# Kernel tuning notes

Measured on AMD Instinct MI355X. Metric: run time of the kernel, lower is better.

The kernel has to match this reference:

```python
import jax, jax.numpy as jnp
import numpy as np

B, C, H, W = 4, 256, 64, 64
CI = 128  # inter_channels = in_channels // 2
EPS = 1e-5  # torch BatchNorm default eps


def setup_inputs() -> dict:
    key = jax.random.key(0)
    ks = jax.random.split(key, 8)

    def w(k, shape, s=0.02):
        return jax.random.normal(k, shape, jnp.float32) * s

    return {
        "x": jax.random.normal(ks[0], (B, C, H, W), jnp.float32),
        # theta (Q) linear + BatchNorm1d (inference-mode running stats)
        "theta_w": w(ks[1], (CI, C)), "theta_b": jnp.zeros((CI,), jnp.float32),
        "theta_bn_gamma": jnp.ones((CI,), jnp.float32), "theta_bn_beta": jnp.zeros((CI,), jnp.float32),
        "theta_bn_mean": jnp.zeros((CI,), jnp.float32), "theta_bn_var": jnp.ones((CI,), jnp.float32),
        # phi (K) linear + BatchNorm1d
        "phi_w": w(ks[2], (CI, C)), "phi_b": jnp.zeros((CI,), jnp.float32),
        "phi_bn_gamma": jnp.ones((CI,), jnp.float32), "phi_bn_beta": jnp.zeros((CI,), jnp.float32),
        "phi_bn_mean": jnp.zeros((CI,), jnp.float32), "phi_bn_var": jnp.ones((CI,), jnp.float32),
        # g (V) linear
        "g_w": w(ks[3], (CI, C)), "g_b": jnp.zeros((CI,), jnp.float32),
        # W_z output linear
        "wz_w": w(ks[4], (C, CI)), "wz_b": jnp.zeros((C,), jnp.float32),
        # output BatchNorm2d (gamma nonzero instead of init-0 so output is non-trivial)
        "bn_gamma": w(ks[5], (C,), 0.1), "bn_beta": jnp.zeros((C,), jnp.float32),
        "bn_mean": jnp.zeros((C,), jnp.float32), "bn_var": jnp.ones((C,), jnp.float32),
    }


def _linear(z, w, b):
    # z: [B, N, C], w: [D, C] -> [B, N, D]
    return jnp.einsum('bnc,dc->bnd', z, w) + b


def _bn(z, gamma, beta, mean, var):
    # per-channel affine BN in inference mode, channel on last axis
    return (z - mean) * jax.lax.rsqrt(var + EPS) * gamma + beta


def reference(x, theta_w, theta_b, theta_bn_gamma, theta_bn_beta, theta_bn_mean, theta_bn_var,
              phi_w, phi_b, phi_bn_gamma, phi_bn_beta, phi_bn_mean, phi_bn_var,
              g_w, g_b, wz_w, wz_b, bn_gamma, bn_beta, bn_mean, bn_var):
    b, c, h, w = x.shape
    n = h * w
    ci = theta_w.shape[0]
    scale = float(ci) ** (-0.5)

    x_flat = x.reshape(b, c, n).transpose(0, 2, 1)  # [B, N, C]
    Q = _bn(_linear(x_flat, theta_w, theta_b), theta_bn_gamma, theta_bn_beta, theta_bn_mean, theta_bn_var)
    K = _bn(_linear(x_flat, phi_w, phi_b), phi_bn_gamma, phi_bn_beta, phi_bn_mean, phi_bn_var)
    V = _linear(x_flat, g_w, g_b)  # [B, N, CI]

    # attention computed in fp32 (matches torch amp-disabled block)
    attn = jnp.einsum('bnd,bmd->bnm', Q.astype(jnp.float32), K.astype(jnp.float32)) * scale
    attn = jax.nn.softmax(attn, axis=-1).astype(V.dtype)  # [B, N, N]

    y = jnp.einsum('bnm,bmd->bnd', attn, V)  # [B, N, CI]
    y = jnp.einsum('bnd,cd->bnc', y, wz_w) + wz_b  # [B, N, C]
    y = y.transpose(0, 2, 1).reshape(b, c, h, w)

    # BatchNorm2d (inference mode), channel axis 1
    rstd = jax.lax.rsqrt(bn_var + EPS)
    y = (y - bn_mean[None, :, None, None]) * (rstd * bn_gamma)[None, :, None, None] + bn_beta[None, :, None, None]
    return y + x
```

## Files before the change

### kernel.cpp

```cpp
#include <hip/hip_runtime.h>
#include <stdint.h>

typedef __attribute__((ext_vector_type(8))) short bf16x8;
typedef __attribute__((ext_vector_type(4))) float f32x4;

#define WS_WQKV   0u
#define WS_WZ     196608u
#define WS_SCL    262144u
#define WS_SHF    263680u
#define WS_WZS    265216u
#define WS_WZT    266240u
#define WS_Q      524288u
#define WS_K      (WS_Q  + 4194304u)
#define WS_VT     (WS_K  + 4194304u)
#define WS_Y      (WS_VT + 4194304u)
#define WS_OP     (WS_Y  + 4194304u)
#define WS_LP     (WS_OP + 16777216u)

__device__ __forceinline__ short f2bf(float f) {
  union { float f; uint32_t u; } v; v.f = f;
  uint32_t r = v.u + 0x7fffu + ((v.u >> 16) & 1u);
  return (short)(r >> 16);
}

__device__ __forceinline__ uint32_t pack2_bf16(float a, float b) {
  union { float f; uint32_t u; } x, y; x.f = a; y.f = b;
  return ((y.u + 0x8000u) & 0xffff0000u) | ((x.u + 0x8000u) >> 16);
}

__device__ __forceinline__ f32x4 mfma16(bf16x8 a, bf16x8 b, f32x4 c) {
  return __builtin_amdgcn_mfma_f32_16x16x32_bf16(a, b, c, 0, 0, 0);
}

__device__ __forceinline__ void load_lds16(const short* gp, short* lp) {
  __builtin_amdgcn_global_load_lds(
      (const __attribute__((address_space(1))) uint32_t*)gp,
      (__attribute__((address_space(3))) uint32_t*)lp, 16, 0, 0);
}

__global__ __launch_bounds__(256) void prep_kernel(
    const float* theta_w, const float* phi_w, const float* g_w, const float* wz_w,
    const float* theta_b, const float* tg, const float* tb, const float* tm, const float* tv,
    const float* phi_b,   const float* pg, const float* pb, const float* pm, const float* pv,
    const float* g_b,
    const float* wz_b, const float* bg, const float* bb, const float* bm, const float* bv,
    char* ws) {
  int idx = blockIdx.x * 256 + threadIdx.x;
  short* wqkv = (short*)(ws + WS_WQKV);
  if (idx < 98304) {
    float w;
    if (idx < 32768) w = theta_w[idx];
    else if (idx < 65536) w = phi_w[idx - 32768];
    else w = g_w[idx - 65536];
    wqkv[idx] = f2bf(w);
  }
  if (idx < 32768) ((short*)(ws + WS_WZ))[idx] = f2bf(wz_w[idx]);
  if (idx < 384) {
    float s, t;
    if (idx < 128)      { s = tg[idx] * rsqrtf(tv[idx] + 1e-5f);
                          t = (theta_b[idx] - tm[idx]) * s + tb[idx]; }
    else if (idx < 256) { int d = idx - 128; s = pg[d] * rsqrtf(pv[d] + 1e-5f);
                          t = (phi_b[d] - pm[d]) * s + pb[d]; }
    else                { int d = idx - 256; s = 1.0f; t = g_b[d]; }
    ((float*)(ws + WS_SCL))[idx] = s;
    ((float*)(ws + WS_SHF))[idx] = t;
  }
  if (idx < 256) {
    float s = bg[idx] * rsqrtf(bv[idx] + 1e-5f);
    float t = (wz_b[idx] - bm[idx]) * s + bb[idx];
    ((float*)(ws + WS_WZS))[idx] = s;
    ((float*)(ws + WS_WZT))[idx] = t;
  }
}

__global__ __launch_bounds__(256) void qkv_kernel(const float* __restrict__ x, char* ws) {
  const int nt2 = blockIdx.x, b = blockIdx.y;
  const int t = threadIdx.x;
  __shared__ __attribute__((aligned(16))) short xs[32][264];
  const short* wqkv = (const short*)(ws + WS_WQKV);
  const float* scl = (const float*)(ws + WS_SCL);
  const float* shf = (const float*)(ws + WS_SHF);
  const int n0 = nt2 * 32;
  #pragma unroll
  for (int i = 0; i < 8; ++i) {
    int chunk = i * 256 + t;
    int c = chunk >> 3, n4 = chunk & 7;
    const float4 v = *(const float4*)(x + ((size_t)(b * 256 + c) << 12) + n0 + n4 * 4);
    xs[n4 * 4 + 0][c] = f2bf(v.x);
    xs[n4 * 4 + 1][c] = f2bf(v.y);
    xs[n4 * 4 + 2][c] = f2bf(v.z);
    xs[n4 * 4 + 3][c] = f2bf(v.w);
  }
  __syncthreads();
  const int wv = t >> 6, l = t & 63, lr = l & 15, q = l >> 4;
  const int wn = wv & 1, dh = wv >> 1;
  bf16x8 a[8];
  #pragma unroll
  for (int kt = 0; kt < 8; ++kt) a[kt] = *(const bf16x8*)&xs[wn * 16 + lr][kt * 32 + q * 8];
  f32x4 acc[12] = {};
  #pragma unroll
  for (int kt = 0; kt < 8; ++kt) {
    #pragma unroll
    for (int s = 0; s < 12; ++s) {
      const short* wp = wqkv + (size_t)(dh * 192 + s * 16 + lr) * 256 + kt * 32 + q * 8;
      bf16x8 bf = *(const bf16x8*)wp;
      acc[s] = mfma16(a[kt], bf, acc[s]);
    }
  }
  const float s2 = 0.08838834764831845f * 1.4426950408889634f;
  #pragma unroll
  for (int s = 0; s < 12; ++s) {
    int dg = dh * 192 + s * 16 + lr;
    float sc = scl[dg], sh = shf[dg];
    if (dg < 128) { sc *= s2; sh *= s2; }
    short vals[4];
    #pragma unroll
    for (int r = 0; r < 4; ++r) vals[r] = f2bf(acc[s][r] * sc + sh);
    int nbase = n0 + wn * 16 + q * 4;
    if (dg < 128) {
      short* Q = (short*)(ws + WS_Q) + ((size_t)b << 19);
      #pragma unroll
      for (int r = 0; r < 4; ++r) Q[(size_t)(nbase + r) * 128 + dg] = vals[r];
    } else if (dg < 256) {
      int d = dg - 128;
      short* Kt = (short*)(ws + WS_K) + ((size_t)b << 19);
      int kt2 = d >> 5, qa = (d >> 3) & 3, e = d & 7;
      int tile = nbase >> 6, sg = (nbase >> 4) & 3, lr0 = nbase & 15;
      size_t base = ((size_t)((tile * 16 + sg * 4 + kt2) * 64 + qa * 16 + lr0) << 3) + e;
      #pragma unroll
      for (int r = 0; r < 4; ++r) Kt[base + r * 8] = vals[r];
    } else {
      int d = dg - 256;
      short* Vt = (short*)(ws + WS_VT) + ((size_t)b << 19);
      int dt = d >> 4, lrv = d & 15;
      int tile = nbase >> 6, mm = nbase & 63;
      int h = mm >> 5, qv = (mm >> 3) & 3, e0 = mm & 7;
      size_t base = ((size_t)((tile * 16 + dt * 2 + h) * 64 + qv * 16 + lrv) << 3) + e0;
      short4 pk; pk.x = vals[0]; pk.y = vals[1]; pk.z = vals[2]; pk.w = vals[3];
      *(short4*)(Vt + base) = pk;
    }
  }
}

__global__ __launch_bounds__(256, 2) void attn_kernel(char* ws) {
  const int g = blockIdx.x;
  const int b = (g & 7) >> 1;
  const int idx = ((g >> 3) << 1) | (g & 1);
  const int nt = idx >> 2, mc = idx & 3;
  const int t = threadIdx.x, w = t >> 6, l = t & 63, lr = l & 15, q = l >> 4;
  __shared__ __attribute__((aligned(16))) short ksl[16][512];
  __shared__ __attribute__((aligned(16))) short vsl[16][512];
  __shared__ __attribute__((aligned(16))) short psl[4][2][2][512];
  const short* Q  = (const short*)(ws + WS_Q)  + ((size_t)b << 19);
  const short* Kt = (const short*)(ws + WS_K)  + ((size_t)b << 19);
  const short* Vt = (const short*)(ws + WS_VT) + ((size_t)b << 19);
  const int n0w = nt * 128 + w * 32;
  bf16x8 qf[2][4];
  #pragma unroll
  for (int j = 0; j < 2; ++j) {
    const short* qp = Q + (size_t)(n0w + j * 16 + lr) * 128 + q * 8;
    #pragma unroll
    for (int kt = 0; kt < 4; ++kt) qf[j][kt] = *(const bf16x8*)(qp + kt * 32);
  }
  f32x4 o[2][8] = {};
  float lsum[2] = {0.f, 0.f};

  for (int it = 0; it < 16; ++it) {
    const int tile = mc * 16 + it;
    const short* kg = Kt + (size_t)tile * 8192;
    const short* vg = Vt + (size_t)tile * 8192;
    __syncthreads();
    #pragma unroll
    for (int i = 0; i < 4; ++i) {
      int gi = i * 4 + w;
      load_lds16(kg + gi * 512 + l * 8, &ksl[gi][0]);
      load_lds16(vg + gi * 512 + l * 8, &vsl[gi][0]);
    }
    __syncthreads();
    f32x4 sacc[2][4] = {};
    #pragma unroll
    for (int kt = 0; kt < 4; ++kt) {
      #pragma unroll
      for (int s = 0; s < 4; ++s) {
        bf16x8 kf = *(const bf16x8*)&ksl[s * 4 + kt][l * 8];
        sacc[0][s] = mfma16(kf, qf[0][kt], sacc[0][s]);
        sacc[1][s] = mfma16(kf, qf[1][kt], sacc[1][s]);
      }
    }
    #pragma unroll
    for (int j = 0; j < 2; ++j) {
      #pragma unroll
      for (int s = 0; s < 4; ++s) {
        float e0 = exp2f(sacc[j][s][0]);
        float e1 = exp2f(sacc[j][s][1]);
        float e2 = exp2f(sacc[j][s][2]);
        float e3 = exp2f(sacc[j][s][3]);
        lsum[j] += (e0 + e1) + (e2 + e3);
        uint2 pk;
        pk.x = pack2_bf16(e0, e1);
        pk.y = pack2_bf16(e2, e3);
        *(uint2*)&psl[w][j][s >> 1][(((s & 1) * 2 + (q >> 1)) * 16 + lr) * 8 + (q & 1) * 4] = pk;
      }
    }
    bf16x8 pf[2][2];
    #pragma unroll
    for (int j = 0; j < 2; ++j)
      #pragma unroll
      for (int h = 0; h < 2; ++h)
        pf[j][h] = *(const bf16x8*)&psl[w][j][h][l * 8];
    #pragma unroll
    for (int dt = 0; dt < 8; ++dt) {
      #pragma unroll
      for (int h = 0; h < 2; ++h) {
        bf16x8 vf = *(const bf16x8*)&vsl[dt * 2 + h][l * 8];
        o[0][dt] = mfma16(vf, pf[0][h], o[0][dt]);
        o[1][dt] = mfma16(vf, pf[1][h], o[1][dt]);
      }
    }
  }
  const int cb = mc * 4 + b;
  float* LP = (float*)(ws + WS_LP) + ((size_t)cb << 12);
  #pragma unroll
  for (int j = 0; j < 2; ++j) {
    float s = lsum[j];
    s += __shfl_xor(s, 16, 64);
    s += __shfl_xor(s, 32, 64);
    if (l < 16) LP[n0w + j * 16 + l] = s;
  }
  short* OPc = (short*)(ws + WS_OP) + ((size_t)cb << 19);
  #pragma unroll
  for (int j = 0; j < 2; ++j)
    #pragma unroll
    for (int dt = 0; dt < 8; ++dt) {
      short4 pk;
      pk.x = f2bf(o[j][dt][0]); pk.y = f2bf(o[j][dt][1]);
      pk.z = f2bf(o[j][dt][2]); pk.w = f2bf(o[j][dt][3]);
      *(short4*)&OPc[((size_t)(n0w + j * 16 + lr) << 7) + dt * 16 + q * 4] = pk;
    }
}

__global__ __launch_bounds__(256) void proj_kernel(const float* __restrict__ x,
                                                   char* ws, float* __restrict__ out) {
  const int nt = blockIdx.x, b = blockIdx.y;
  const int t = threadIdx.x, wv = t >> 6, l = t & 63, lr = l & 15, q = l >> 4;
  __shared__ __attribute__((aligned(16))) short ys[16][136];
  const short* OP = (const short*)(ws + WS_OP);
  const float* LP = (const float*)(ws + WS_LP);
  const short* WZ = (const short*)(ws + WS_WZ);
  const float* wzs = (const float*)(ws + WS_WZS);
  const float* wzt = (const float*)(ws + WS_WZT);
  const int n0 = nt * 16;
  {
    int row = t >> 4, d8 = (t & 15) * 8;
    int n = n0 + row;
    float acc8[8] = {};
    float lsf = 0.f;
    #pragma unroll
    for (int mc = 0; mc < 4; ++mc) {
      int cb = mc * 4 + b;
      const short* p = OP + ((size_t)cb << 19) + ((size_t)n << 7) + d8;
      uint4 v = *(const uint4*)p;
      uint32_t uu[4] = {v.x, v.y, v.z, v.w};
      #pragma unroll
      for (int w = 0; w < 4; ++w) {
        union { uint32_t u; float f; } lo, hi;
        lo.u = uu[w] << 16; hi.u = uu[w] & 0xffff0000u;
        acc8[w * 2 + 0] += lo.f;
        acc8[w * 2 + 1] += hi.f;
      }
      lsf += LP[(cb << 12) + n];
    }
    float inv = 1.0f / lsf;
    short out8[8];
    #pragma unroll
    for (int j = 0; j < 8; ++j) out8[j] = f2bf(acc8[j] * inv);
    *(uint4*)&ys[row][d8] = *(uint4*)out8;
  }
  __syncthreads();
  bf16x8 a[4];
  #pragma unroll
  for (int kt = 0; kt < 4; ++kt) a[kt] = *(const bf16x8*)&ys[lr][kt * 32 + q * 8];
  f32x4 acc[4] = {};
  #pragma unroll
  for (int kt = 0; kt < 4; ++kt) {
    #pragma unroll
    for (int s = 0; s < 4; ++s) {
      const short* wp = WZ + (size_t)(wv * 64 + s * 16 + lr) * 128 + kt * 32 + q * 8;
      bf16x8 bf = *(const bf16x8*)wp;
      acc[s] = mfma16(a[kt], bf, acc[s]);
    }
  }
  #pragma unroll
  for (int s = 0; s < 4; ++s) {
    int c = wv * 64 + s * 16 + lr;
    float sc = wzs[c], sh = wzt[c];
    int nbase = n0 + q * 4;
    size_t base = ((size_t)(b * 256 + c) << 12) + nbase;
    float4 xv = *(const float4*)(x + base);
    float4 ov;
    ov.x = acc[s][0] * sc + sh + xv.x;
    ov.y = acc[s][1] * sc + sh + xv.y;
    ov.z = acc[s][2] * sc + sh + xv.z;
    ov.w = acc[s][3] * sc + sh + xv.w;
    *(float4*)(out + base) = ov;
  }
}

extern "C" void kernel_launch(void* const* d_in, const int* in_sizes, int n_in,
                              void* d_out, int out_size, void* d_ws, size_t ws_size,
                              hipStream_t stream) {
  const float* x       = (const float*)d_in[0];
  const float* theta_w = (const float*)d_in[1];
  const float* theta_b = (const float*)d_in[2];
  const float* tg      = (const float*)d_in[3];
  const float* tb      = (const float*)d_in[4];
  const float* tm      = (const float*)d_in[5];
  const float* tv      = (const float*)d_in[6];
  const float* phi_w   = (const float*)d_in[7];
  const float* phi_b   = (const float*)d_in[8];
  const float* pg      = (const float*)d_in[9];
  const float* pb      = (const float*)d_in[10];
  const float* pm      = (const float*)d_in[11];
  const float* pv      = (const float*)d_in[12];
  const float* g_w     = (const float*)d_in[13];
  const float* g_b     = (const float*)d_in[14];
  const float* wz_w    = (const float*)d_in[15];
  const float* wz_b    = (const float*)d_in[16];
  const float* bg      = (const float*)d_in[17];
  const float* bb      = (const float*)d_in[18];
  const float* bm      = (const float*)d_in[19];
  const float* bv      = (const float*)d_in[20];
  char* ws = (char*)d_ws;
  float* out = (float*)d_out;

  prep_kernel<<<384, 256, 0, stream>>>(theta_w, phi_w, g_w, wz_w,
                                       theta_b, tg, tb, tm, tv,
                                       phi_b, pg, pb, pm, pv,
                                       g_b, wz_b, bg, bb, bm, bv, ws);
  qkv_kernel<<<dim3(128, 4), 256, 0, stream>>>(x, ws);
  attn_kernel<<<512, 256, 0, stream>>>(ws);
  proj_kernel<<<dim3(256, 4), 256, 0, stream>>>(x, ws, out);
}
```

Measured before the change: 196.6 us.

## Double-buffer K/V LDS tiles in attention loop and raise MFMA wave priority

The attention kernel now keeps two LDS buffers for K and V. The next tile's global-to-LDS copy is issued before computing on the current tile, with one barrier per tile instead of two, so memory latency can overlap with MFMA work. s_setprio brackets the MFMA sections to favour waves issuing matrix ops. LDS use per block grows from about 48KB to about 80KB, which may limit how many blocks fit on a CU alongside the two-blocks-per-CU launch bound.

```diff
diff --git a/kernel.cpp b/kernel.cpp
--- a/kernel.cpp
+++ b/kernel.cpp
@@ -148,8 +148,10 @@
   const int idx = ((g >> 3) << 1) | (g & 1);
   const int nt = idx >> 2, mc = idx & 3;
   const int t = threadIdx.x, w = t >> 6, l = t & 63, lr = l & 15, q = l >> 4;
-  __shared__ __attribute__((aligned(16))) short ksl[16][512];
-  __shared__ __attribute__((aligned(16))) short vsl[16][512];
+  __shared__ __attribute__((aligned(16))) short ks0[16][512];
+  __shared__ __attribute__((aligned(16))) short vs0[16][512];
+  __shared__ __attribute__((aligned(16))) short ks1[16][512];
+  __shared__ __attribute__((aligned(16))) short vs1[16][512];
   __shared__ __attribute__((aligned(16))) short psl[4][2][2][512];
   const short* Q  = (const short*)(ws + WS_Q)  + ((size_t)b << 19);
   const short* Kt = (const short*)(ws + WS_K)  + ((size_t)b << 19);
@@ -165,19 +167,23 @@
   f32x4 o[2][8] = {};
   float lsum[2] = {0.f, 0.f};
 
-  for (int it = 0; it < 16; ++it) {
-    const int tile = mc * 16 + it;
-    const short* kg = Kt + (size_t)tile * 8192;
-    const short* vg = Vt + (size_t)tile * 8192;
-    __syncthreads();
+  const short* kbase = Kt + (size_t)(mc * 16) * 8192;
+  const short* vbase = Vt + (size_t)(mc * 16) * 8192;
+
+  auto stage = [&](short (*KS)[512], short (*VS)[512], int it) {
+    const short* kg = kbase + (size_t)it * 8192;
+    const short* vg = vbase + (size_t)it * 8192;
     #pragma unroll
     for (int i = 0; i < 4; ++i) {
       int gi = i * 4 + w;
-      load_lds16(kg + gi * 512 + l * 8, &ksl[gi][0]);
-      load_lds16(vg + gi * 512 + l * 8, &vsl[gi][0]);
-    }
-    __syncthreads();
+      load_lds16(kg + gi * 512 + l * 8, &KS[gi][0]);
+      load_lds16(vg + gi * 512 + l * 8, &VS[gi][0]);
+    }
+  };
+
+  auto compute = [&](short (*ksl)[512], short (*vsl)[512]) {
     f32x4 sacc[2][4] = {};
+    __builtin_amdgcn_s_setprio(1);
     #pragma unroll
     for (int kt = 0; kt < 4; ++kt) {
       #pragma unroll
@@ -187,6 +193,7 @@
         sacc[1][s] = mfma16(kf, qf[1][kt], sacc[1][s]);
       }
     }
+    __builtin_amdgcn_s_setprio(0);
     #pragma unroll
     for (int j = 0; j < 2; ++j) {
       #pragma unroll
@@ -208,6 +215,7 @@
       #pragma unroll
       for (int h = 0; h < 2; ++h)
         pf[j][h] = *(const bf16x8*)&psl[w][j][h][l * 8];
+    __builtin_amdgcn_s_setprio(1);
     #pragma unroll
     for (int dt = 0; dt < 8; ++dt) {
       #pragma unroll
@@ -217,7 +225,20 @@
         o[1][dt] = mfma16(vf, pf[1][h], o[1][dt]);
       }
     }
-  }
+    __builtin_amdgcn_s_setprio(0);
+  };
+
+  stage(ks0, vs0, 0);
+  __syncthreads();
+  for (int it2 = 0; it2 < 8; ++it2) {
+    stage(ks1, vs1, it2 * 2 + 1);
+    compute(ks0, vs0);
+    __syncthreads();
+    if (it2 < 7) stage(ks0, vs0, it2 * 2 + 2);
+    compute(ks1, vs1);
+    __syncthreads();
+  }
+
   const int cb = mc * 4 + b;
   float* LP = (float*)(ws + WS_LP) + ((size_t)cb << 12);
   #pragma unroll
```

Result: no change. 200.0 us (+1.8%).

## Halve attention query tile per block, double grid, raise occupancy, add setprio

Applied to the files above, without the earlier changes.

Each attention block now handles 64 query rows instead of 128, so each wave owns 16 rows. The grid doubles to 1024 blocks, the probability scratch in shared memory shrinks, and launch bounds now request 4 blocks per CU. The aim is more resident waves to hide the latency of LDS, exp and global loads, and s_setprio is raised around the MFMA sections to favour matrix issue. The cost is that each loaded K/V fragment now feeds one MFMA instead of two, which doubles K/V traffic from L2 and LDS per unit of work.

```diff
diff --git a/kernel.cpp b/kernel.cpp
--- a/kernel.cpp
+++ b/kernel.cpp
@@ -142,7 +142,7 @@
   }
 }
 
-__global__ __launch_bounds__(256, 2) void attn_kernel(char* ws) {
+__global__ __launch_bounds__(256, 4) void attn_kernel(char* ws) {
   const int g = blockIdx.x;
   const int b = (g & 7) >> 1;
   const int idx = ((g >> 3) << 1) | (g & 1);
@@ -150,20 +150,19 @@
   const int t = threadIdx.x, w = t >> 6, l = t & 63, lr = l & 15, q = l >> 4;
   __shared__ __attribute__((aligned(16))) short ksl[16][512];
   __shared__ __attribute__((aligned(16))) short vsl[16][512];
-  __shared__ __attribute__((aligned(16))) short psl[4][2][2][512];
+  __shared__ __attribute__((aligned(16))) short psl[4][2][512];
   const short* Q  = (const short*)(ws + WS_Q)  + ((size_t)b << 19);
   const short* Kt = (const short*)(ws + WS_K)  + ((size_t)b << 19);
   const short* Vt = (const short*)(ws + WS_VT) + ((size_t)b << 19);
-  const int n0w = nt * 128 + w * 32;
-  bf16x8 qf[2][4];
-  #pragma unroll
-  for (int j = 0; j < 2; ++j) {
-    const short* qp = Q + (size_t)(n0w + j * 16 + lr) * 128 + q * 8;
-    #pragma unroll
-    for (int kt = 0; kt < 4; ++kt) qf[j][kt] = *(const bf16x8*)(qp + kt * 32);
-  }
-  f32x4 o[2][8] = {};
-  float lsum[2] = {0.f, 0.f};
+  const int n0w = nt * 64 + w * 16;
+  bf16x8 qf[4];
+  {
+    const short* qp = Q + (size_t)(n0w + lr) * 128 + q * 8;
+    #pragma unroll
+    for (int kt = 0; kt < 4; ++kt) qf[kt] = *(const bf16x8*)(qp + kt * 32);
+  }
+  f32x4 o[8] = {};
+  float lsum = 0.f;
 
   for (int it = 0; it < 16; ++it) {
     const int tile = mc * 16 + it;
@@ -177,66 +176,60 @@
       load_lds16(vg + gi * 512 + l * 8, &vsl[gi][0]);
     }
     __syncthreads();
-    f32x4 sacc[2][4] = {};
+    f32x4 sacc[4] = {};
+    __builtin_amdgcn_s_setprio(1);
     #pragma unroll
     for (int kt = 0; kt < 4; ++kt) {
       #pragma unroll
       for (int s = 0; s < 4; ++s) {
         bf16x8 kf = *(const bf16x8*)&ksl[s * 4 + kt][l * 8];
-        sacc[0][s] = mfma16(kf, qf[0][kt], sacc[0][s]);
-        sacc[1][s] = mfma16(kf, qf[1][kt], sacc[1][s]);
+        sacc[s] = mfma16(kf, qf[kt], sacc[s]);
       }
     }
-    #pragma unroll
-    for (int j = 0; j < 2; ++j) {
-      #pragma unroll
-      for (int s = 0; s < 4; ++s) {
-        float e0 = exp2f(sacc[j][s][0]);
-        float e1 = exp2f(sacc[j][s][1]);
-        float e2 = exp2f(sacc[j][s][2]);
-        float e3 = exp2f(sacc[j][s][3]);
-        lsum[j] += (e0 + e1) + (e2 + e3);
-        uint2 pk;
-        pk.x = pack2_bf16(e0, e1);
-        pk.y = pack2_bf16(e2, e3);
-        *(uint2*)&psl[w][j][s >> 1][(((s & 1) * 2 + (q >> 1)) * 16 + lr) * 8 + (q & 1) * 4] = pk;
-      }
-    }
-    bf16x8 pf[2][2];
-    #pragma unroll
-    for (int j = 0; j < 2; ++j)
-      #pragma unroll
-      for (int h = 0; h < 2; ++h)
-        pf[j][h] = *(const bf16x8*)&psl[w][j][h][l * 8];
+    __builtin_amdgcn_s_setprio(0);
+    #pragma unroll
+    for (int s = 0; s < 4; ++s) {
+      float e0 = exp2f(sacc[s][0]);
+      float e1 = exp2f(sacc[s][1]);
+      float e2 = exp2f(sacc[s][2]);
+      float e3 = exp2f(sacc[s][3]);
+      lsum += (e0 + e1) + (e2 + e3);
+      uint2 pk;
+      pk.x = pack2_bf16(e0, e1);
+      pk.y = pack2_bf16(e2, e3);
+      *(uint2*)&psl[w][s >> 1][(((s & 1) * 2 + (q >> 1)) * 16 + lr) * 8 + (q & 1) * 4] = pk;
+    }
+    bf16x8 pf[2];
+    #pragma unroll
+    for (int h = 0; h < 2; ++h)
+      pf[h] = *(const bf16x8*)&psl[w][h][l * 8];
+    __builtin_amdgcn_s_setprio(1);
     #pragma unroll
     for (int dt = 0; dt < 8; ++dt) {
       #pragma unroll
       for (int h = 0; h < 2; ++h) {
         bf16x8 vf = *(const bf16x8*)&vsl[dt * 2 + h][l * 8];
-        o[0][dt] = mfma16(vf, pf[0][h], o[0][dt]);
-        o[1][dt] = mfma16(vf, pf[1][h], o[1][dt]);
+        o[dt] = mfma16(vf, pf[h], o[dt]);
       }
     }
+    __builtin_amdgcn_s_setprio(0);
   }
   const int cb = mc * 4 + b;
   float* LP = (float*)(ws + WS_LP) + ((size_t)cb << 12);
-  #pragma unroll
-  for (int j = 0; j < 2; ++j) {
-    float s = lsum[j];
+  {
+    float s = lsum;
     s += __shfl_xor(s, 16, 64);
     s += __shfl_xor(s, 32, 64);
-    if (l < 16) LP[n0w + j * 16 + l] = s;
+    if (l < 16) LP[n0w + l] = s;
   }
   short* OPc = (short*)(ws + WS_OP) + ((size_t)cb << 19);
   #pragma unroll
-  for (int j = 0; j < 2; ++j)
-    #pragma unroll
-    for (int dt = 0; dt < 8; ++dt) {
-      short4 pk;
-      pk.x = f2bf(o[j][dt][0]); pk.y = f2bf(o[j][dt][1]);
-      pk.z = f2bf(o[j][dt][2]); pk.w = f2bf(o[j][dt][3]);
-      *(short4*)&OPc[((size_t)(n0w + j * 16 + lr) << 7) + dt * 16 + q * 4] = pk;
-    }
+  for (int dt = 0; dt < 8; ++dt) {
+    short4 pk;
+    pk.x = f2bf(o[dt][0]); pk.y = f2bf(o[dt][1]);
+    pk.z = f2bf(o[dt][2]); pk.w = f2bf(o[dt][3]);
+    *(short4*)&OPc[((size_t)(n0w + lr) << 7) + dt * 16 + q * 4] = pk;
+  }
 }
 
 __global__ __launch_bounds__(256) void proj_kernel(const float* __restrict__ x,
@@ -338,6 +331,6 @@
                                        phi_b, pg, pb, pm, pv,
                                        g_b, wz_b, bg, bb, bm, bv, ws);
   qkv_kernel<<<dim3(128, 4), 256, 0, stream>>>(x, ws);
-  attn_kernel<<<512, 256, 0, stream>>>(ws);
+  attn_kernel<<<1024, 256, 0, stream>>>(ws);
   proj_kernel<<<dim3(256, 4), 256, 0, stream>>>(x, ws, out);
 }
```

After: 199.0 us. No clear change (+1.2%).
